# Performance work log

Measured on AMD Instinct MI355X. Metric: run time of the kernel, lower is better.

The kernel has to match this reference:

```python
import jax, jax.numpy as jnp
import numpy as np

C_IN, C_OUT, KH, KW = 64, 128, 3, 3
STRIDE, PAD, DIL = 1, 1, 1
EPS = 1e-5


def setup_inputs() -> dict:
    key = jax.random.key(0)
    ks = jax.random.split(key, 7)
    B, H, W = 8, 112, 112
    x = jax.random.normal(ks[0], (B, C_IN, H, W), dtype=jnp.float32)
    # offset conv: produces 2*KH*KW offset channels; small init keeps offsets sane
    w_off = jax.random.normal(ks[1], (2 * KH * KW, C_IN, KH, KW), dtype=jnp.float32) * 0.01
    b_off = jax.random.normal(ks[2], (2 * KH * KW,), dtype=jnp.float32) * 0.01
    # deformable conv weight/bias
    fan_in = C_IN * KH * KW
    w_dcn = jax.random.normal(ks[3], (C_OUT, C_IN, KH, KW), dtype=jnp.float32) / np.sqrt(fan_in)
    b_dcn = jax.random.normal(ks[4], (C_OUT,), dtype=jnp.float32) * 0.01
    gamma = jnp.ones((C_OUT,), dtype=jnp.float32)
    beta = jnp.zeros((C_OUT,), dtype=jnp.float32)
    return {"x": x, "w_off": w_off, "b_off": b_off, "w_dcn": w_dcn,
            "b_dcn": b_dcn, "gamma": gamma, "beta": beta}


def _conv2d(x, w, b):
    y = jax.lax.conv_general_dilated(
        x, w, window_strides=(STRIDE, STRIDE),
        padding=((PAD, PAD), (PAD, PAD)),
        rhs_dilation=(DIL, DIL),
        dimension_numbers=("NCHW", "OIHW", "NCHW"))
    return y + b[None, :, None, None]


def _deform_conv(x, offset, w, b):
    # x: [B,C,H,W]; offset: [B, 2*KH*KW, Ho, Wo] with (dy, dx) pairs per tap
    B, C, H, W = x.shape
    KK = KH * KW
    Ho, Wo = offset.shape[2], offset.shape[3]
    off = offset.reshape(B, KK, 2, Ho, Wo)
    ky = (jnp.arange(KK) // KW).astype(jnp.float32)  # kernel row per tap
    kx = (jnp.arange(KK) % KW).astype(jnp.float32)
    base_y = (jnp.arange(Ho) * STRIDE - PAD).astype(jnp.float32)
    base_x = (jnp.arange(Wo) * STRIDE - PAD).astype(jnp.float32)
    # sampling positions [B, KK, Ho, Wo]
    py = off[:, :, 0] + base_y[None, None, :, None] + (ky * DIL)[None, :, None, None]
    px = off[:, :, 1] + base_x[None, None, None, :] + (kx * DIL)[None, :, None, None]

    y0 = jnp.floor(py)
    x0 = jnp.floor(px)
    wy1 = py - y0  # weight for y0+1
    wx1 = px - x0
    y0i = y0.astype(jnp.int32)
    x0i = x0.astype(jnp.int32)

    x_flat = x.reshape(B, C, H * W)

    def gather_corner(yi, xi, wgt):
        # yi, xi, wgt: [B, KK, Ho, Wo]
        valid = (yi >= 0) & (yi < H) & (xi >= 0) & (xi < W)
        idx = jnp.clip(yi, 0, H - 1) * W + jnp.clip(xi, 0, W - 1)
        idx = idx.reshape(B, -1)  # [B, KK*Ho*Wo]
        vals = jnp.take_along_axis(x_flat, idx[:, None, :], axis=2)  # [B, C, N]
        coef = (wgt * valid.astype(wgt.dtype)).reshape(B, 1, -1)
        return vals * coef

    samp = (gather_corner(y0i,     x0i,     (1 - wy1) * (1 - wx1))
            + gather_corner(y0i,     x0i + 1, (1 - wy1) * wx1)
            + gather_corner(y0i + 1, x0i,     wy1 * (1 - wx1))
            + gather_corner(y0i + 1, x0i + 1, wy1 * wx1))
    samp = samp.reshape(B, C, KK, Ho, Wo)
    out = jnp.einsum("bckhw,ock->bohw", samp, w.reshape(w.shape[0], C, KK))
    return out + b[None, :, None, None]


def reference(x, w_off, b_off, w_dcn, b_dcn, gamma, beta):
    offset = _conv2d(x, w_off, b_off)
    y = _deform_conv(x, offset, w_dcn, b_dcn)
    # BatchNorm2d (training mode: biased batch stats) + ReLU
    mean = jnp.mean(y, axis=(0, 2, 3))
    var = jnp.var(y, axis=(0, 2, 3))
    yhat = (y - mean[None, :, None, None]) * jax.lax.rsqrt(var + EPS)[None, :, None, None]
    y = gamma[None, :, None, None] * yhat + beta[None, :, None, None]
    return jax.nn.relu(y)
```

## Files before the change

### kernel.cpp

```cpp
#include <hip/hip_runtime.h>

#define H    112
#define W    112
#define HW   12544
#define CIN  64
#define COUT 128
#define BATCH 8
#define KK   9
#define OFFC 18
#define EPS  1e-5f
#define TP   32
#define KDIM 576
#define KHALF 288
#define KPAD2 296

typedef unsigned short ushort;
typedef unsigned int uint;
typedef __attribute__((ext_vector_type(8))) short short8;
typedef __attribute__((ext_vector_type(8))) ushort ushort8;
typedef __attribute__((ext_vector_type(4))) float floatx4;

__device__ __forceinline__ ushort f2bf(float f) {
  uint u = __float_as_uint(f);
  u = (u + 0x7FFFu + ((u >> 16) & 1u)) >> 16;
  return (ushort)u;
}

__device__ __forceinline__ uint pack_bf2(float f0, float f1) {
  uint u0 = __float_as_uint(f0) + 0x8000u;
  uint u1 = __float_as_uint(f1) + 0x8000u;
  return __builtin_amdgcn_perm(u1, u0, 0x07060302u);
}

__device__ __forceinline__ float bf2f(ushort u) {
  return __uint_as_float(((uint)u) << 16);
}

__global__ __launch_bounds__(256) void k_transpose_x(
    const float* __restrict__ x, ushort* __restrict__ xTb) {
  __shared__ float tile[64][65];
  int b = blockIdx.y;
  int p0 = blockIdx.x * 64;
  int tid = threadIdx.x;
  int j = tid & 63, cb = tid >> 6;
#pragma unroll
  for (int i = 0; i < 16; ++i) {
    int ci = cb * 16 + i;
    tile[ci][j] = x[((size_t)(b * CIN + ci)) * HW + p0 + j];
  }
  __syncthreads();
  int px = tid >> 2, ciq = tid & 3;
#pragma unroll
  for (int g = 0; g < 4; ++g) {
    int ci = ciq * 16 + g * 4;
    uint lo = pack_bf2(tile[ci + 0][px], tile[ci + 1][px]);
    uint hi = pack_bf2(tile[ci + 2][px], tile[ci + 3][px]);
    *(uint2*)&xTb[((size_t)b * HW + p0 + px) * 64 + ci] = make_uint2(lo, hi);
  }
}

__global__ __launch_bounds__(256) void k_prep_w(
    const float* __restrict__ w_off, const float* __restrict__ w_dcn,
    ushort* __restrict__ w_offT, ushort* __restrict__ w_mf) {
  int i = blockIdx.x * 256 + threadIdx.x;
  if (i < 32 * KDIM) {
    int oc = i / KDIM, k = i - oc * KDIM;
    int kk = k >> 6, ci = k & 63;
    float v = (oc < OFFC) ? w_off[(oc * CIN + ci) * KK + kk] : 0.f;
    w_offT[i] = f2bf(v);
  } else if (i < 32 * KDIM + COUT * KDIM) {
    int jj = i - 32 * KDIM;
    int co = jj / KDIM, k = jj - co * KDIM;
    int h = k / KHALF, r = k - h * KHALF;
    int kk = r >> 5, cil = r & 31;
    int ci = h * 32 + cil;
    w_mf[jj] = f2bf(w_dcn[(co * CIN + ci) * KK + kk]);
  }
}

__global__ __launch_bounds__(256) void k_offset_conv(
    const ushort* __restrict__ xTb, const ushort* __restrict__ w_offT,
    const float* __restrict__ bias, float* __restrict__ out) {
  int b = blockIdx.y;
  int wave = threadIdx.x >> 6, lane = threadIdx.x & 63;
  int row16 = lane & 15, quad = lane >> 4;
  int p = blockIdx.x * 64 + wave * 16 + row16;
  int ho = p / W, wo = p - ho * W;
  const ushort* xb = xTb + (size_t)b * HW * 64;

  short8 Bf[18];
#pragma unroll
  for (int ks = 0; ks < 18; ++ks) {
    int kk = ks >> 1;
    int ci0 = (ks & 1) * 32 + quad * 8;
    int kh = kk / 3, kw = kk - kh * 3;
    int yy = ho + kh - 1, xx = wo + kw - 1;
    bool valid = (yy >= 0) & (yy < H) & (xx >= 0) & (xx < W);
    short8 v = {0, 0, 0, 0, 0, 0, 0, 0};
    if (valid) v = *(const short8*)(xb + ((size_t)(yy * W + xx) << 6) + ci0);
    Bf[ks] = v;
  }
  floatx4 acc0 = {0.f, 0.f, 0.f, 0.f}, acc1 = acc0;
  const ushort* wa0 = w_offT + row16 * KDIM + quad * 8;
  const ushort* wa1 = w_offT + (16 + row16) * KDIM + quad * 8;
#pragma unroll
  for (int ks = 0; ks < 18; ++ks) {
    short8 A0 = *(const short8*)(wa0 + ks * 32);
    short8 A1 = *(const short8*)(wa1 + ks * 32);
    acc0 = __builtin_amdgcn_mfma_f32_16x16x32_bf16(A0, Bf[ks], acc0, 0, 0, 0);
    acc1 = __builtin_amdgcn_mfma_f32_16x16x32_bf16(A1, Bf[ks], acc1, 0, 0, 0);
  }
  float* ob = out + (size_t)b * OFFC * HW;
#pragma unroll
  for (int reg = 0; reg < 4; ++reg) {
    int oc = quad * 4 + reg;
    ob[(size_t)oc * HW + p] = acc0[reg] + bias[oc];
    int oc1 = 16 + oc;
    if (oc1 < OFFC) ob[(size_t)oc1 * HW + p] = acc1[reg] + bias[oc1];
  }
}

__global__ __launch_bounds__(256) void k_deform(
    const ushort* __restrict__ xTb, const float* __restrict__ off,
    const ushort* __restrict__ w_mf, float* __restrict__ y) {
  __shared__ float4 s_w[KK][TP];
  __shared__ int4   s_i[KK][TP];
  __shared__ ushort samp[TP][KPAD2];

  int b = blockIdx.y;
  int p0 = blockIdx.x * TP;
  int tid = threadIdx.x;
  const ushort* xb = xTb + (size_t)b * HW * 64;

  for (int it = tid; it < KK * TP; it += 256) {
    int kk = it >> 5;
    int px = it & 31;
    int p = p0 + px;
    int ho = p / W, wo = p - ho * W;
    float dy = off[((size_t)b * OFFC + 2 * kk) * HW + p];
    float dx = off[((size_t)b * OFFC + 2 * kk + 1) * HW + p];
    float py = dy + (float)(ho - 1 + kk / 3);
    float pxx = dx + (float)(wo - 1 + kk % 3);
    float y0f = floorf(py), x0f = floorf(pxx);
    float wy1 = py - y0f, wx1 = pxx - x0f;
    int y0 = (int)y0f, x0 = (int)x0f;
    int y1 = y0 + 1, x1 = x0 + 1;
    float vy0 = (y0 >= 0 && y0 < H) ? 1.f : 0.f;
    float vy1 = (y1 >= 0 && y1 < H) ? 1.f : 0.f;
    float vx0 = (x0 >= 0 && x0 < W) ? 1.f : 0.f;
    float vx1 = (x1 >= 0 && x1 < W) ? 1.f : 0.f;
    int cy0 = min(max(y0, 0), H - 1), cy1 = min(max(y1, 0), H - 1);
    int cx0 = min(max(x0, 0), W - 1), cx1 = min(max(x1, 0), W - 1);
    s_w[kk][px] = make_float4((1.f - wy1) * (1.f - wx1) * vy0 * vx0,
                              (1.f - wy1) * wx1 * vy0 * vx1,
                              wy1 * (1.f - wx1) * vy1 * vx0,
                              wy1 * wx1 * vy1 * vx1);
    s_i[kk][px] = make_int4((cy0 * W + cx0) << 6, (cy0 * W + cx1) << 6,
                            (cy1 * W + cx0) << 6, (cy1 * W + cx1) << 6);
  }
  __syncthreads();

  int wave = tid >> 6, lane = tid & 63;
  int row16 = lane & 15, quad = lane >> 4;
  int koff = quad * 8;
  int co_base = wave * 32;
  const ushort* wa0 = w_mf + (size_t)(co_base + row16) * KDIM + koff;
  const ushort* wa1 = w_mf + (size_t)(co_base + 16 + row16) * KDIM + koff;

  floatx4 acc00 = {0.f, 0.f, 0.f, 0.f}, acc01 = acc00, acc10 = acc00, acc11 = acc00;

  for (int h = 0; h < 2; ++h) {
#pragma unroll
    for (int r = 0; r < 5; ++r) {
      int it = tid + r * 256;
      if (it < 1152) {
        int px = it / 36;
        int rem = it - px * 36;
        int kk = rem >> 2;
        int cig = rem & 3;
        int cil0 = cig * 8;
        int cio = h * 32 + cil0;
        float4 wv = s_w[kk][px];
        int4 iv = s_i[kk][px];
        ushort8 c0 = *(const ushort8*)(xb + iv.x + cio);
        ushort8 c1 = *(const ushort8*)(xb + iv.y + cio);
        ushort8 c2 = *(const ushort8*)(xb + iv.z + cio);
        ushort8 c3 = *(const ushort8*)(xb + iv.w + cio);
        uint pk[4];
#pragma unroll
        for (int g = 0; g < 4; ++g) {
          float r0 = wv.x * bf2f(c0[2 * g])     + wv.y * bf2f(c1[2 * g]) +
                     wv.z * bf2f(c2[2 * g])     + wv.w * bf2f(c3[2 * g]);
          float r1 = wv.x * bf2f(c0[2 * g + 1]) + wv.y * bf2f(c1[2 * g + 1]) +
                     wv.z * bf2f(c2[2 * g + 1]) + wv.w * bf2f(c3[2 * g + 1]);
          pk[g] = pack_bf2(r0, r1);
        }
        *(uint4*)&samp[px][kk * 32 + cil0] = make_uint4(pk[0], pk[1], pk[2], pk[3]);
      }
    }
    __syncthreads();

    const ushort* sb0 = &samp[row16][koff];
    const ushort* sb1 = &samp[16 + row16][koff];
    const ushort* a0 = wa0 + h * KHALF;
    const ushort* a1 = wa1 + h * KHALF;
#pragma unroll
    for (int ks = 0; ks < 9; ++ks) {
      short8 A0 = *(const short8*)(a0 + ks * 32);
      short8 A1 = *(const short8*)(a1 + ks * 32);
      short8 B0 = *(const short8*)(sb0 + ks * 32);
      short8 B1 = *(const short8*)(sb1 + ks * 32);
      acc00 = __builtin_amdgcn_mfma_f32_16x16x32_bf16(A0, B0, acc00, 0, 0, 0);
      acc01 = __builtin_amdgcn_mfma_f32_16x16x32_bf16(A0, B1, acc01, 0, 0, 0);
      acc10 = __builtin_amdgcn_mfma_f32_16x16x32_bf16(A1, B0, acc10, 0, 0, 0);
      acc11 = __builtin_amdgcn_mfma_f32_16x16x32_bf16(A1, B1, acc11, 0, 0, 0);
    }
    if (h == 0) __syncthreads();
  }

  float* yb = y + (size_t)b * COUT * HW + p0;
#pragma unroll
  for (int reg = 0; reg < 4; ++reg) {
    int r0 = quad * 4 + reg;
    yb[(size_t)(co_base + r0) * HW + row16]      = acc00[reg];
    yb[(size_t)(co_base + r0) * HW + 16 + row16] = acc01[reg];
    yb[(size_t)(co_base + 16 + r0) * HW + row16]      = acc10[reg];
    yb[(size_t)(co_base + 16 + r0) * HW + 16 + row16] = acc11[reg];
  }
}

__global__ __launch_bounds__(256) void k_stats(const float* __restrict__ y,
                                               float* __restrict__ stats) {
  int c = blockIdx.x & 127;
  int half = blockIdx.x >> 7;
  int tid = threadIdx.x;
  float s = 0.f, s2 = 0.f;
#pragma unroll
  for (int bb = 0; bb < 2; ++bb) {
    int b = half * 2 + bb;
    const float4* yp = (const float4*)(y + ((size_t)b * COUT + c) * HW);
    for (int p = tid; p < HW / 4; p += 256) {
      float4 v = yp[p];
      s += v.x + v.y + v.z + v.w;
      s2 += v.x * v.x + v.y * v.y + v.z * v.z + v.w * v.w;
    }
  }
#pragma unroll
  for (int o = 32; o > 0; o >>= 1) {
    s += __shfl_down(s, o, 64);
    s2 += __shfl_down(s2, o, 64);
  }
  __shared__ float ls[4], ls2[4];
  int lane = tid & 63, wid = tid >> 6;
  if (lane == 0) { ls[wid] = s; ls2[wid] = s2; }
  __syncthreads();
  if (tid == 0) {
    atomicAdd(&stats[c], ls[0] + ls[1] + ls[2] + ls[3]);
    atomicAdd(&stats[COUT + c], ls2[0] + ls2[1] + ls2[2] + ls2[3]);
  }
}

__global__ __launch_bounds__(256) void k_norm(const float* __restrict__ y,
                                              const float* __restrict__ stats,
                                              const float* __restrict__ gamma,
                                              const float* __restrict__ beta,
                                              float* __restrict__ out) {
  int i4 = blockIdx.x * 256 + threadIdx.x;
  const int total4 = BATCH * COUT * HW / 4;
  if (i4 >= total4) return;
  size_t i = (size_t)i4 * 4;
  int c = (int)((i / HW) & (COUT - 1));
  const float N = (float)(BATCH * HW);
  float m = stats[c] / N;
  float var = stats[COUT + c] / N - m * m;
  float r = rsqrtf(var + EPS);
  float g = gamma[c], bt = beta[c];
  float4 v = *(const float4*)&y[i];
  v.x = fmaxf(0.f, (v.x - m) * r * g + bt);
  v.y = fmaxf(0.f, (v.y - m) * r * g + bt);
  v.z = fmaxf(0.f, (v.z - m) * r * g + bt);
  v.w = fmaxf(0.f, (v.w - m) * r * g + bt);
  *(float4*)&out[i] = v;
}

extern "C" void kernel_launch(void* const* d_in, const int* in_sizes, int n_in,
                              void* d_out, int out_size, void* d_ws, size_t ws_size,
                              hipStream_t stream) {
  const float* x     = (const float*)d_in[0];
  const float* w_off = (const float*)d_in[1];
  const float* b_off = (const float*)d_in[2];
  const float* w_dcn = (const float*)d_in[3];
  const float* gamma = (const float*)d_in[5];
  const float* beta  = (const float*)d_in[6];
  float* out = (float*)d_out;

  float* ws = (float*)d_ws;
  float*  off_buf = ws;
  float*  y       = off_buf + 1806336;
  float*  stats   = y + 12845056;
  ushort* xTb     = (ushort*)(stats + 256);
  ushort* w_mf    = xTb + 6422528;
  ushort* w_offT  = w_mf + 73728;

  hipMemsetAsync(stats, 0, 256 * sizeof(float), stream);
  k_transpose_x<<<dim3(HW / 64, BATCH), 256, 0, stream>>>(x, xTb);
  k_prep_w<<<(32 * KDIM + COUT * KDIM + 255) / 256, 256, 0, stream>>>(w_off, w_dcn, w_offT, w_mf);
  k_offset_conv<<<dim3(HW / 64, BATCH), 256, 0, stream>>>(xTb, w_offT, b_off, off_buf);
  k_deform<<<dim3(HW / TP, BATCH), 256, 0, stream>>>(xTb, off_buf, w_mf, y);
  k_stats<<<512, 256, 0, stream>>>(y, stats);
  k_norm<<<(BATCH * COUT * HW / 4 + 255) / 256, 256, 0, stream>>>(y, stats, gamma, beta, out);
}
```

Measured before the change: 236.5 us.

## Fuse BN statistics into deform epilogue and store intermediate as bf16

The deformable-conv kernel now computes per-block channel sums and sums of squares from its accumulators with wave shuffles and writes them to a partial-stats buffer. A small deterministic reduce kernel replaces the full-tensor stats pass and the atomics. The intermediate y is stored as bf16 instead of fp32, which halves the write and the read in the norm kernel. In exchange it adds bf16 rounding error on the pre-norm activations, and the norm kernel carries a leftover unused 16-byte load.

```diff
diff --git a/kernel.cpp b/kernel.cpp
--- a/kernel.cpp
+++ b/kernel.cpp
@@ -13,6 +13,7 @@
 #define KDIM 576
 #define KHALF 288
 #define KPAD2 296
+#define NB   3136
 
 typedef unsigned short ushort;
 typedef unsigned int uint;
@@ -122,13 +123,15 @@
 
 __global__ __launch_bounds__(256) void k_deform(
     const ushort* __restrict__ xTb, const float* __restrict__ off,
-    const ushort* __restrict__ w_mf, float* __restrict__ y) {
+    const ushort* __restrict__ w_mf, ushort* __restrict__ y,
+    float* __restrict__ psT) {
   __shared__ float4 s_w[KK][TP];
   __shared__ int4   s_i[KK][TP];
   __shared__ ushort samp[TP][KPAD2];
 
   int b = blockIdx.y;
   int p0 = blockIdx.x * TP;
+  int bid = blockIdx.y * gridDim.x + blockIdx.x;
   int tid = threadIdx.x;
   const ushort* xb = xTb + (size_t)b * HW * 64;
 
@@ -218,49 +221,55 @@
     if (h == 0) __syncthreads();
   }
 
-  float* yb = y + (size_t)b * COUT * HW + p0;
+  ushort* yb = y + (size_t)b * COUT * HW + p0;
 #pragma unroll
   for (int reg = 0; reg < 4; ++reg) {
     int r0 = quad * 4 + reg;
-    yb[(size_t)(co_base + r0) * HW + row16]      = acc00[reg];
-    yb[(size_t)(co_base + r0) * HW + 16 + row16] = acc01[reg];
-    yb[(size_t)(co_base + 16 + r0) * HW + row16]      = acc10[reg];
-    yb[(size_t)(co_base + 16 + r0) * HW + 16 + row16] = acc11[reg];
-  }
-}
-
-__global__ __launch_bounds__(256) void k_stats(const float* __restrict__ y,
-                                               float* __restrict__ stats) {
-  int c = blockIdx.x & 127;
-  int half = blockIdx.x >> 7;
+    yb[(size_t)(co_base + r0) * HW + row16]      = f2bf(acc00[reg]);
+    yb[(size_t)(co_base + r0) * HW + 16 + row16] = f2bf(acc01[reg]);
+    yb[(size_t)(co_base + 16 + r0) * HW + row16]      = f2bf(acc10[reg]);
+    yb[(size_t)(co_base + 16 + r0) * HW + 16 + row16] = f2bf(acc11[reg]);
+  }
+#pragma unroll
+  for (int reg = 0; reg < 4; ++reg) {
+    float s0 = acc00[reg] + acc01[reg];
+    float q0 = acc00[reg] * acc00[reg] + acc01[reg] * acc01[reg];
+    float s1 = acc10[reg] + acc11[reg];
+    float q1 = acc10[reg] * acc10[reg] + acc11[reg] * acc11[reg];
+#pragma unroll
+    for (int m = 1; m < 16; m <<= 1) {
+      s0 += __shfl_xor(s0, m, 64);
+      q0 += __shfl_xor(q0, m, 64);
+      s1 += __shfl_xor(s1, m, 64);
+      q1 += __shfl_xor(q1, m, 64);
+    }
+    if (row16 == 0) {
+      int c0 = co_base + quad * 4 + reg;
+      int c1 = c0 + 16;
+      psT[(size_t)c0 * NB + bid]         = s0;
+      psT[(size_t)(128 + c0) * NB + bid] = q0;
+      psT[(size_t)c1 * NB + bid]         = s1;
+      psT[(size_t)(128 + c1) * NB + bid] = q1;
+    }
+  }
+}
+
+__global__ __launch_bounds__(256) void k_reduce(const float* __restrict__ psT,
+                                                float* __restrict__ stats) {
+  int j = blockIdx.x;
   int tid = threadIdx.x;
-  float s = 0.f, s2 = 0.f;
-#pragma unroll
-  for (int bb = 0; bb < 2; ++bb) {
-    int b = half * 2 + bb;
-    const float4* yp = (const float4*)(y + ((size_t)b * COUT + c) * HW);
-    for (int p = tid; p < HW / 4; p += 256) {
-      float4 v = yp[p];
-      s += v.x + v.y + v.z + v.w;
-      s2 += v.x * v.x + v.y * v.y + v.z * v.z + v.w * v.w;
-    }
-  }
-#pragma unroll
-  for (int o = 32; o > 0; o >>= 1) {
-    s += __shfl_down(s, o, 64);
-    s2 += __shfl_down(s2, o, 64);
-  }
-  __shared__ float ls[4], ls2[4];
+  float s = 0.f;
+  for (int i = tid; i < NB; i += 256) s += psT[(size_t)j * NB + i];
+#pragma unroll
+  for (int o = 32; o > 0; o >>= 1) s += __shfl_down(s, o, 64);
+  __shared__ float ls[4];
   int lane = tid & 63, wid = tid >> 6;
-  if (lane == 0) { ls[wid] = s; ls2[wid] = s2; }
+  if (lane == 0) ls[wid] = s;
   __syncthreads();
-  if (tid == 0) {
-    atomicAdd(&stats[c], ls[0] + ls[1] + ls[2] + ls[3]);
-    atomicAdd(&stats[COUT + c], ls2[0] + ls2[1] + ls2[2] + ls2[3]);
-  }
-}
-
-__global__ __launch_bounds__(256) void k_norm(const float* __restrict__ y,
+  if (tid == 0) stats[j] = ls[0] + ls[1] + ls[2] + ls[3];
+}
+
+__global__ __launch_bounds__(256) void k_norm(const ushort* __restrict__ y,
                                               const float* __restrict__ stats,
                                               const float* __restrict__ gamma,
                                               const float* __restrict__ beta,
@@ -275,7 +284,11 @@
   float var = stats[COUT + c] / N - m * m;
   float r = rsqrtf(var + EPS);
   float g = gamma[c], bt = beta[c];
-  float4 v = *(const float4*)&y[i];
+  ushort8 v8 = *(const ushort8*)&y[i];
+  uint2 u = *(const uint2*)&y[i];
+  float4 v = make_float4(bf2f((ushort)(u.x & 0xFFFF)), bf2f((ushort)(u.x >> 16)),
+                         bf2f((ushort)(u.y & 0xFFFF)), bf2f((ushort)(u.y >> 16)));
+  (void)v8;
   v.x = fmaxf(0.f, (v.x - m) * r * g + bt);
   v.y = fmaxf(0.f, (v.y - m) * r * g + bt);
   v.z = fmaxf(0.f, (v.z - m) * r * g + bt);
@@ -296,17 +309,17 @@
 
   float* ws = (float*)d_ws;
   float*  off_buf = ws;
-  float*  y       = off_buf + 1806336;
-  float*  stats   = y + 12845056;
+  float*  psT     = off_buf + 1806336;
+  float*  stats   = psT + 802816;
   ushort* xTb     = (ushort*)(stats + 256);
   ushort* w_mf    = xTb + 6422528;
   ushort* w_offT  = w_mf + 73728;
-
-  hipMemsetAsync(stats, 0, 256 * sizeof(float), stream);
+  ushort* y_bf    = w_offT + 18432;
+
   k_transpose_x<<<dim3(HW / 64, BATCH), 256, 0, stream>>>(x, xTb);
   k_prep_w<<<(32 * KDIM + COUT * KDIM + 255) / 256, 256, 0, stream>>>(w_off, w_dcn, w_offT, w_mf);
   k_offset_conv<<<dim3(HW / 64, BATCH), 256, 0, stream>>>(xTb, w_offT, b_off, off_buf);
-  k_deform<<<dim3(HW / TP, BATCH), 256, 0, stream>>>(xTb, off_buf, w_mf, y);
-  k_stats<<<512, 256, 0, stream>>>(y, stats);
-  k_norm<<<(BATCH * COUT * HW / 4 + 255) / 256, 256, 0, stream>>>(y, stats, gamma, beta, out);
-}
+  k_deform<<<dim3(HW / TP, BATCH), 256, 0, stream>>>(xTb, off_buf, w_mf, y_bf, psT);
+  k_reduce<<<256, 256, 0, stream>>>(psT, stats);
+  k_norm<<<(BATCH * COUT * HW / 4 + 255) / 256, 256, 0, stream>>>(y_bf, stats, gamma, beta, out);
+}
```

After: 227.6 us. 1.04x faster.
